# Kernel tuning notes

Hardware: AMD Instinct MI355X
Metric: run time of the kernel (lower is better)

Reference implementation:

```python
import jax, jax.numpy as jnp
import numpy as np

# CogForge GroupedQueryAttention (prefill path): GQA + RoPE + sliding-window+global-token mask
B, T, DM = 2, 2048, 768
H, HKV, DH = 12, 4, 64          # d_head = d_model // n_heads
GROUPS = H // HKV               # kv_groups = 3
WIN, GLB = 512, 64              # window_size, global_tokens
THETA = 10000.0


def _rotate_half(x):
    half = x.shape[-1] // 2
    return jnp.concatenate([-x[..., half:], x[..., :half]], axis=-1)


def _rope_cos_sin(seq_len, dim, dtype):
    inv_freq = 1.0 / (THETA ** (jnp.arange(0, dim, 2, dtype=jnp.float32) / dim))
    t = jnp.arange(seq_len, dtype=jnp.float32)
    freqs = jnp.outer(t, inv_freq)                      # [T, DH/2]
    emb = jnp.concatenate([freqs, freqs], axis=-1)      # [T, DH]
    return jnp.cos(emb).astype(dtype)[None, None], jnp.sin(emb).astype(dtype)[None, None]


def _sparse_mask(seq_len):
    # allowed(i,j) = causal AND (within window OR j is a global token)
    i = jnp.arange(seq_len)[:, None]
    j = jnp.arange(seq_len)[None, :]
    allowed = (j <= i) & (((i - j) < WIN) | (j < GLB))
    return jnp.where(allowed, 0.0, -jnp.inf).astype(jnp.float32)  # [T, T]


def setup_inputs() -> dict:
    key = jax.random.key(0)
    kx, kq, kk, kv, ko = jax.random.split(key, 5)
    x = jax.random.normal(kx, (B, T, DM), jnp.float32)
    wq = jax.random.normal(kq, (DM, H * DH), jnp.float32) * 0.02
    wk = jax.random.normal(kk, (DM, HKV * DH), jnp.float32) * 0.02
    wv = jax.random.normal(kv, (DM, HKV * DH), jnp.float32) * 0.02
    wo = jax.random.normal(ko, (H * DH, DM), jnp.float32) * 0.02
    return {"x": x, "wq": wq, "wk": wk, "wv": wv, "wo": wo}


def reference(x, wq, wk, wv, wo):
    # projections -> [B, heads, T, DH]
    q = (x @ wq).reshape(B, T, H, DH).transpose(0, 2, 1, 3)
    k = (x @ wk).reshape(B, T, HKV, DH).transpose(0, 2, 1, 3)
    v = (x @ wv).reshape(B, T, HKV, DH).transpose(0, 2, 1, 3)

    cos, sin = _rope_cos_sin(T, DH, x.dtype)            # [1,1,T,DH]
    q = q * cos + _rotate_half(q) * sin
    k = k * cos + _rotate_half(k) * sin

    # expand kv heads to match query heads (GQA)
    k = jnp.repeat(k, GROUPS, axis=1)                   # [B,H,T,DH]
    v = jnp.repeat(v, GROUPS, axis=1)

    scale = 1.0 / jnp.sqrt(jnp.asarray(DH, x.dtype))
    scores = jnp.einsum('bhtd,bhsd->bhts', q, k) * scale
    scores = scores + _sparse_mask(T)[None, None]
    weights = jax.nn.softmax(scores, axis=-1)           # attn_dropout = 0.0

    out = jnp.einsum('bhts,bhsd->bhtd', weights, v)
    out = out.transpose(0, 2, 1, 3).reshape(B, T, H * DH)
    return out @ wo
```

## Files before the change

kernel.cpp:

```cpp
#include <hip/hip_runtime.h>
#include <hip/hip_bf16.h>


typedef __attribute__((ext_vector_type(8))) short bf16x8;
typedef __attribute__((ext_vector_type(4))) short bf16x4;
typedef __attribute__((ext_vector_type(4))) float f32x4;
typedef __attribute__((ext_vector_type(4))) unsigned short u16x4;

#define MFMA   __builtin_amdgcn_mfma_f32_16x16x32_bf16
#define MFMA16 __builtin_amdgcn_mfma_f32_16x16x16bf16_1k

constexpr int BB = 2, TT = 2048, DM = 768, HH = 12, HKV = 4, DH = 64;
constexpr int WIN = 512, GLB = 64;
constexpr float SC2 = 0.18033688011112042f;

__device__ __forceinline__ unsigned short f2b(float f) {
    union { float f; unsigned int u; } v; v.f = f;
    unsigned int r = v.u + 0x7fffu + ((v.u >> 16) & 1u);
    return (unsigned short)(r >> 16);
}

#define GLOAD_LDS(gp, lp)                                                      \
    __builtin_amdgcn_global_load_lds(                                          \
        (const __attribute__((address_space(1))) void*)(gp),                   \
        (__attribute__((address_space(3))) void*)(lp), 16, 0, 0)

__global__ __launch_bounds__(256) void k_pre(const float* __restrict__ x,
                                             unsigned short* __restrict__ xb,
                                             float2* __restrict__ rope,
                                             const float* __restrict__ wq,
                                             const float* __restrict__ wk,
                                             const float* __restrict__ wv,
                                             const float* __restrict__ wo,
                                             unsigned short* __restrict__ wqT,
                                             unsigned short* __restrict__ wkT,
                                             unsigned short* __restrict__ wvT,
                                             unsigned short* __restrict__ woT) {
    __shared__ float t[32][33];
    int bid = blockIdx.x, tid = threadIdx.x;
    if (bid < 3072) {
        int i = bid * 256 + tid;
        float4 v = ((const float4*)x)[i];
        u16x4 o; o.x = f2b(v.x); o.y = f2b(v.y); o.z = f2b(v.z); o.w = f2b(v.w);
        ((u16x4*)xb)[i] = o;
        return;
    }
    if (bid < 3328) {
        int i = (bid - 3072) * 256 + tid;
        int tt = i >> 5, p = i & 31;
        float inv = exp2f(-(float)p * (13.287712379549449f / 32.0f));
        float ang = (float)tt * inv;
        rope[i] = make_float2(cosf(ang), sinf(ang));
        return;
    }
    int wb = bid - 3328;
    const float* src; unsigned short* dst; int N, tile;
    if (wb < 576)      { src = wq; dst = wqT; N = 768; tile = wb; }
    else if (wb < 768) { src = wk; dst = wkT; N = 256; tile = wb - 576; }
    else if (wb < 960) { src = wv; dst = wvT; N = 256; tile = wb - 768; }
    else               { src = wo; dst = woT; N = 768; tile = wb - 960; }
    int ntiles = N / 32;
    int k0 = (tile / ntiles) * 32, n0 = (tile % ntiles) * 32;
    int tx = tid & 31, ty = tid >> 5;
    #pragma unroll
    for (int e = 0; e < 4; ++e) {
        int r = ty + e * 8;
        t[r][tx] = src[(size_t)(k0 + r) * N + n0 + tx];
    }
    __syncthreads();
    #pragma unroll
    for (int e = 0; e < 4; ++e) {
        int r = ty + e * 8;
        dst[(size_t)(n0 + r) * DM + k0 + tx] = f2b(t[tx][r]);
    }
}

__global__ __launch_bounds__(256) void k_qkv(const unsigned short* __restrict__ xb,
                                             const unsigned short* __restrict__ wqT,
                                             const unsigned short* __restrict__ wkT,
                                             const unsigned short* __restrict__ wvT,
                                             unsigned short* __restrict__ qb,
                                             unsigned short* __restrict__ kb,
                                             unsigned short* __restrict__ vtb,
                                             const float2* __restrict__ rope) {
    __shared__ __align__(16) unsigned short Ab[2][64 * 64];
    __shared__ __align__(16) unsigned short Bb[2][64 * 64];
    const int tid = threadIdx.x;
    const int wave = tid >> 6, lane = tid & 63;
    const int quad = lane >> 4, col = lane & 15;
    const int y = blockIdx.y;
    int mode, hl;
    const unsigned short* Bt;
    if (y < 12)      { mode = 0; hl = y;      Bt = wqT + (size_t)hl * 64 * DM; }
    else if (y < 16) { mode = 1; hl = y - 12; Bt = wkT + (size_t)hl * 64 * DM; }
    else             { mode = 2; hl = y - 16; Bt = wvT + (size_t)hl * 64 * DM; }
    const int m0b = blockIdx.x * 64;

    const int rg = lane >> 3;
    const int cg = (lane & 7) ^ rg;
    const int ck = col & 7;

    f32x4 acc[4];
    #pragma unroll
    for (int j = 0; j < 4; ++j) acc[j] = f32x4{0.f, 0.f, 0.f, 0.f};

    auto stage = [&](int buf, int k) {
        #pragma unroll
        for (int m = 0; m < 2; ++m) {
            int g = wave * 2 + m;
            GLOAD_LDS(xb + (size_t)(m0b + g * 8 + rg) * DM + k + cg * 8,
                      &Ab[buf][g * 512]);
        }
        #pragma unroll
        for (int m = 0; m < 2; ++m) {
            int g = wave * 2 + m;
            GLOAD_LDS(Bt + (size_t)(g * 8 + rg) * DM + k + cg * 8,
                      &Bb[buf][g * 512]);
        }
    };

    stage(0, 0);
    __syncthreads();

    const int arow = (wave * 16 + col) * 64;

    for (int t = 0; t < 12; ++t) {
        const int buf = t & 1;
        if (t < 11) stage(buf ^ 1, (t + 1) * 64);
        __builtin_amdgcn_s_setprio(1);
        #pragma unroll
        for (int ks = 0; ks < 2; ++ks) {
            const int p = ((ks * 4 + quad) ^ ck) * 8;
            bf16x8 a = *(const bf16x8*)&Ab[buf][arow + p];
            #pragma unroll
            for (int j = 0; j < 4; ++j) {
                bf16x8 b = *(const bf16x8*)&Bb[buf][(j * 16 + col) * 64 + p];
                acc[j] = MFMA(a, b, acc[j], 0, 0, 0);
            }
        }
        __builtin_amdgcn_s_setprio(0);
        __syncthreads();
    }

    if (mode == 2) {
        int b = m0b >> 11;
        #pragma unroll
        for (int j = 0; j < 4; ++j)
            #pragma unroll
            for (int r = 0; r < 4; ++r) {
                int m = m0b + wave * 16 + quad * 4 + r;
                int t = m & (TT - 1);
                int d = j * 16 + col;
                vtb[((size_t)(b * HKV + hl) * DH + d) * TT + t] = f2b(acc[j][r]);
            }
        return;
    }
    int nheads = (mode == 0) ? HH : HKV;
    unsigned short* ob = (mode == 0) ? qb : kb;
    #pragma unroll
    for (int r = 0; r < 4; ++r) {
        int m = m0b + wave * 16 + quad * 4 + r;
        int t = m & (TT - 1);
        int b = m >> 11;
        float2 cs0 = rope[t * 32 + col];
        float2 cs1 = rope[t * 32 + 16 + col];
        float v0 = acc[0][r], v1 = acc[1][r], v2 = acc[2][r], v3 = acc[3][r];
        unsigned short* dst = ob + ((size_t)(b * nheads + hl) * TT + t) * DH + col;
        dst[0]  = f2b(v0 * cs0.x - v2 * cs0.y);
        dst[16] = f2b(v1 * cs1.x - v3 * cs1.y);
        dst[32] = f2b(v2 * cs0.x + v0 * cs0.y);
        dst[48] = f2b(v3 * cs1.x + v1 * cs1.y);
    }
}

__global__ __launch_bounds__(256) void k_out(const unsigned short* __restrict__ ao,
                                             const unsigned short* __restrict__ woT,
                                             float* __restrict__ out) {
    __shared__ __align__(16) unsigned short Ab[2][64 * 64];
    __shared__ __align__(16) unsigned short Bb[2][64 * 64];
    const int tid = threadIdx.x;
    const int wave = tid >> 6, lane = tid & 63;
    const int quad = lane >> 4, col = lane & 15;
    const int m0b = blockIdx.x * 64;
    const int n0 = blockIdx.y * 64;

    const int rg = lane >> 3;
    const int cg = (lane & 7) ^ rg;
    const int ck = col & 7;

    f32x4 acc[4];
    #pragma unroll
    for (int j = 0; j < 4; ++j) acc[j] = f32x4{0.f, 0.f, 0.f, 0.f};

    auto stage = [&](int buf, int k) {
        #pragma unroll
        for (int m = 0; m < 2; ++m) {
            int g = wave * 2 + m;
            GLOAD_LDS(ao + (size_t)(m0b + g * 8 + rg) * DM + k + cg * 8,
                      &Ab[buf][g * 512]);
        }
        #pragma unroll
        for (int m = 0; m < 2; ++m) {
            int g = wave * 2 + m;
            GLOAD_LDS(woT + (size_t)(n0 + g * 8 + rg) * DM + k + cg * 8,
                      &Bb[buf][g * 512]);
        }
    };

    stage(0, 0);
    __syncthreads();

    const int arow = (wave * 16 + col) * 64;

    for (int t = 0; t < 12; ++t) {
        const int buf = t & 1;
        if (t < 11) stage(buf ^ 1, (t + 1) * 64);
        __builtin_amdgcn_s_setprio(1);
        #pragma unroll
        for (int ks = 0; ks < 2; ++ks) {
            const int p = ((ks * 4 + quad) ^ ck) * 8;
            bf16x8 a = *(const bf16x8*)&Ab[buf][arow + p];
            #pragma unroll
            for (int j = 0; j < 4; ++j) {
                bf16x8 b = *(const bf16x8*)&Bb[buf][(j * 16 + col) * 64 + p];
                acc[j] = MFMA(a, b, acc[j], 0, 0, 0);
            }
        }
        __builtin_amdgcn_s_setprio(0);
        __syncthreads();
    }

    #pragma unroll
    for (int j = 0; j < 4; ++j)
        #pragma unroll
        for (int r = 0; r < 4; ++r) {
            int m = m0b + wave * 16 + quad * 4 + r;
            out[(size_t)m * DM + n0 + j * 16 + col] = acc[j][r];
        }
}

__global__ __launch_bounds__(256) void k_attn(const unsigned short* __restrict__ Q,
                                              const unsigned short* __restrict__ K,
                                              const unsigned short* __restrict__ Vt,
                                              unsigned short* __restrict__ AO) {
    __shared__ __align__(16) unsigned short kbuf[2][64 * 64];
    __shared__ __align__(16) unsigned short vbuf[2][64 * 64];
    const int lane = threadIdx.x & 63;
    const int wave = threadIdx.x >> 6;
    const int quad = lane >> 4, col = lane & 15;
    const int lbid = (blockIdx.x & 7) * 96 + (blockIdx.x >> 3);
    const int qb = lbid & 31, bh = lbid >> 5;
    const int h = bh % HH, b = bh / HH;
    const int hkv = h / 3;
    const int i0 = qb * 64 + wave * 16;
    const int irow = i0 + col;

    const unsigned short* qbase = Q + ((size_t)(b * HH + h) * TT + irow) * DH + quad * 8;
    const bf16x8 qf0 = *(const bf16x8*)qbase;
    const bf16x8 qf1 = *(const bf16x8*)(qbase + 32);
    const unsigned short* kbase = K + (size_t)(b * HKV + hkv) * TT * DH;
    const unsigned short* vbase = Vt + (size_t)(b * HKV + hkv) * DH * TT;

    float m_run = -1e30f, l_lane = 0.f;
    f32x4 accO[4];
    #pragma unroll
    for (int dt = 0; dt < 4; ++dt) accO[dt] = f32x4{0.f, 0.f, 0.f, 0.f};

    int jw0 = (qb * 64 - WIN + 1) & ~63; if (jw0 < 64) jw0 = 64;
    const int jlast = qb * 64;
    const int nt = 1 + ((jlast >= 64) ? (((jlast - jw0) >> 6) + 1) : 0);
    auto j0_of = [&](int t) { return (t == 0) ? 0 : (jw0 + ((t - 1) << 6)); };

    const int sr = lane >> 3;
    const int soff = ((lane & 7) ^ sr) * 8;
    const int ck = col & 7;

    auto stage = [&](int bb, int j0) {
        GLOAD_LDS(kbase + (size_t)(j0 + wave * 16 + sr) * DH + soff,
                  &kbuf[bb][(wave * 16) * 64]);
        GLOAD_LDS(kbase + (size_t)(j0 + wave * 16 + 8 + sr) * DH + soff,
                  &kbuf[bb][(wave * 16 + 8) * 64]);
        GLOAD_LDS(vbase + (size_t)(wave * 16 + sr) * TT + j0 + soff,
                  &vbuf[bb][(wave * 16) * 64]);
        GLOAD_LDS(vbase + (size_t)(wave * 16 + 8 + sr) * TT + j0 + soff,
                  &vbuf[bb][(wave * 16 + 8) * 64]);
    };

    stage(0, 0);
    __syncthreads();

    for (int t = 0; t < nt; ++t) {
        const int bb = t & 1;
        if (t + 1 < nt) stage(bb ^ 1, j0_of(t + 1));

        const int j0 = j0_of(t);
        const int mode = (t == 0) ? ((i0 < 64) ? 1 : 0)
                       : (((j0 + 63 > i0) || (j0 <= i0 + 15 - WIN)) ? 2 : 0);

        f32x4 sT[4];
        #pragma unroll
        for (int f = 0; f < 4; ++f) sT[f] = f32x4{0.f, 0.f, 0.f, 0.f};
        __builtin_amdgcn_s_setprio(1);
        #pragma unroll
        for (int f = 0; f < 4; ++f) {
            bf16x8 k0 = *(const bf16x8*)&kbuf[bb][(f * 16 + col) * 64 + (quad ^ ck) * 8];
            bf16x8 k1 = *(const bf16x8*)&kbuf[bb][(f * 16 + col) * 64 + ((4 + quad) ^ ck) * 8];
            sT[f] = MFMA(k0, qf0, sT[f], 0, 0, 0);
            sT[f] = MFMA(k1, qf1, sT[f], 0, 0, 0);
        }
        __builtin_amdgcn_s_setprio(0);

        const int dq = irow - j0 - quad * 4;
        if (mode == 1) {
            #pragma unroll
            for (int f = 0; f < 4; ++f)
                #pragma unroll
                for (int r = 0; r < 4; ++r)
                    if (dq - f * 16 - r < 0) sT[f][r] = -3e30f;
        } else if (mode == 2) {
            #pragma unroll
            for (int f = 0; f < 4; ++f)
                #pragma unroll
                for (int r = 0; r < 4; ++r)
                    if ((unsigned)(dq - f * 16 - r) >= (unsigned)WIN) sT[f][r] = -3e30f;
        }

        float mx = -3e30f;
        #pragma unroll
        for (int f = 0; f < 4; ++f)
            #pragma unroll
            for (int r = 0; r < 4; ++r) mx = fmaxf(mx, sT[f][r]);

        if (!__all(mx <= m_run + 44.f)) {
            float rm = fmaxf(mx, __shfl_xor(mx, 16));
            rm = fmaxf(rm, __shfl_xor(rm, 32));
            float mn = fmaxf(m_run, rm);
            float corr = exp2f((m_run - mn) * SC2);
            m_run = mn;
            l_lane *= corr;
            #pragma unroll
            for (int dt = 0; dt < 4; ++dt)
                #pragma unroll
                for (int r = 0; r < 4; ++r) accO[dt][r] *= corr;
        }

        const float mbase = m_run * SC2;
        unsigned int pk[4][2];
        float ps = 0.f;
        #pragma unroll
        for (int f = 0; f < 4; ++f) {
            float p0 = exp2f(__builtin_fmaf(sT[f][0], SC2, -mbase));
            float p1 = exp2f(__builtin_fmaf(sT[f][1], SC2, -mbase));
            float p2 = exp2f(__builtin_fmaf(sT[f][2], SC2, -mbase));
            float p3 = exp2f(__builtin_fmaf(sT[f][3], SC2, -mbase));
            ps += (p0 + p1) + (p2 + p3);
            asm("v_cvt_pk_bf16_f32 %0, %1, %2" : "=v"(pk[f][0]) : "v"(p0), "v"(p1));
            asm("v_cvt_pk_bf16_f32 %0, %1, %2" : "=v"(pk[f][1]) : "v"(p2), "v"(p3));
        }
        l_lane += ps;

        __builtin_amdgcn_s_setprio(1);
        #pragma unroll
        for (int f = 0; f < 4; ++f) {
            union { bf16x4 v; unsigned int u[2]; } pb;
            pb.u[0] = pk[f][0];
            pb.u[1] = pk[f][1];
            const int voff = (((2 * f + (quad >> 1)) ^ ck) << 3) + ((quad & 1) << 2);
            #pragma unroll
            for (int dt = 0; dt < 4; ++dt) {
                bf16x4 va = *(const bf16x4*)&vbuf[bb][(dt * 16 + col) * 64 + voff];
                accO[dt] = MFMA16(va, pb.v, accO[dt], 0, 0, 0);
            }
        }
        __builtin_amdgcn_s_setprio(0);

        __syncthreads();
    }

    float lr = l_lane;
    lr += __shfl_xor(lr, 16);
    lr += __shfl_xor(lr, 32);
    const float inv = 1.0f / lr;

    unsigned short* dst = AO + ((size_t)b * TT + irow) * DM + h * DH + quad * 4;
    #pragma unroll
    for (int dt = 0; dt < 4; ++dt) {
        u16x4 o;
        o.x = f2b(accO[dt][0] * inv);
        o.y = f2b(accO[dt][1] * inv);
        o.z = f2b(accO[dt][2] * inv);
        o.w = f2b(accO[dt][3] * inv);
        *(u16x4*)(dst + dt * 16) = o;
    }
}

extern "C" void kernel_launch(void* const* d_in, const int* in_sizes, int n_in,
                              void* d_out, int out_size, void* d_ws, size_t ws_size,
                              hipStream_t stream) {
    const float* x  = (const float*)d_in[0];
    const float* wq = (const float*)d_in[1];
    const float* wk = (const float*)d_in[2];
    const float* wv = (const float*)d_in[3];
    const float* wo = (const float*)d_in[4];
    float* out = (float*)d_out;

    char* ws = (char*)d_ws;
    size_t off = 0;
    auto alloc = [&](size_t bytes) -> void* {
        void* p = ws + off;
        off += (bytes + 255) & ~(size_t)255;
        return p;
    };
    const int M = BB * TT;
    unsigned short* xb  = (unsigned short*)alloc((size_t)M * DM * 2);
    unsigned short* wqT = (unsigned short*)alloc((size_t)DM * DM * 2);
    unsigned short* wkT = (unsigned short*)alloc((size_t)(HKV * DH) * DM * 2);
    unsigned short* wvT = (unsigned short*)alloc((size_t)(HKV * DH) * DM * 2);
    unsigned short* woT = (unsigned short*)alloc((size_t)DM * DM * 2);
    unsigned short* qb  = (unsigned short*)alloc((size_t)BB * HH * TT * DH * 2);
    unsigned short* kb  = (unsigned short*)alloc((size_t)BB * HKV * TT * DH * 2);
    unsigned short* vtb = (unsigned short*)alloc((size_t)BB * HKV * DH * TT * 2);
    unsigned short* ao  = (unsigned short*)alloc((size_t)M * DM * 2);
    float2* rope        = (float2*)alloc((size_t)TT * 32 * sizeof(float2));

    k_pre<<<4864, 256, 0, stream>>>(x, xb, rope, wq, wk, wv, wo, wqT, wkT, wvT, woT);
    k_qkv<<<dim3(M / 64, 20), 256, 0, stream>>>(xb, wqT, wkT, wvT, qb, kb, vtb, rope);
    k_attn<<<768, 256, 0, stream>>>(qb, kb, vtb, ao);
    k_out<<<dim3(M / 64, 12), 256, 0, stream>>>(ao, woT, out);
}
```

Measured before the change: 63.89 us.

## Retile QKV and output GEMMs to 128x128 blocks with 2x2 wave grid

New measurement: 75.41 us. 1.18x slower.

```diff
diff --git a/kernel.cpp b/kernel.cpp
--- a/kernel.cpp
+++ b/kernel.cpp
@@ -83,160 +83,165 @@
                                              unsigned short* __restrict__ kb,
                                              unsigned short* __restrict__ vtb,
                                              const float2* __restrict__ rope) {
-    __shared__ __align__(16) unsigned short Ab[2][64 * 64];
-    __shared__ __align__(16) unsigned short Bb[2][64 * 64];
+    __shared__ __align__(16) unsigned short Ab[2][128 * 32];
+    __shared__ __align__(16) unsigned short Bb[2][128 * 32];
     const int tid = threadIdx.x;
     const int wave = tid >> 6, lane = tid & 63;
     const int quad = lane >> 4, col = lane & 15;
+    const int wr = wave >> 1, wc = wave & 1;
     const int y = blockIdx.y;
-    int mode, hl;
+    const int m0b = blockIdx.x * 128;
+    int mode;
     const unsigned short* Bt;
-    if (y < 12)      { mode = 0; hl = y;      Bt = wqT + (size_t)hl * 64 * DM; }
-    else if (y < 16) { mode = 1; hl = y - 12; Bt = wkT + (size_t)hl * 64 * DM; }
-    else             { mode = 2; hl = y - 16; Bt = wvT + (size_t)hl * 64 * DM; }
-    const int m0b = blockIdx.x * 64;
-
-    const int rg = lane >> 3;
-    const int cg = (lane & 7) ^ rg;
-    const int ck = col & 7;
-
-    f32x4 acc[4];
-    #pragma unroll
-    for (int j = 0; j < 4; ++j) acc[j] = f32x4{0.f, 0.f, 0.f, 0.f};
+    int hbase;
+    if (y < 6)      { mode = 0; Bt = wqT + (size_t)(y * 128) * DM;       hbase = y * 2; }
+    else if (y < 8) { mode = 1; Bt = wkT + (size_t)((y - 6) * 128) * DM; hbase = (y - 6) * 2; }
+    else            { mode = 2; Bt = wvT + (size_t)((y - 8) * 128) * DM; hbase = (y - 8) * 2; }
+
+    const int srow = lane >> 2;
+    const int sch  = (lane & 3) * 8;
+
+    f32x4 acc[4][4];
+    #pragma unroll
+    for (int m = 0; m < 4; ++m)
+        #pragma unroll
+        for (int n = 0; n < 4; ++n) acc[m][n] = f32x4{0.f, 0.f, 0.f, 0.f};
 
     auto stage = [&](int buf, int k) {
-        #pragma unroll
-        for (int m = 0; m < 2; ++m) {
-            int g = wave * 2 + m;
-            GLOAD_LDS(xb + (size_t)(m0b + g * 8 + rg) * DM + k + cg * 8,
-                      &Ab[buf][g * 512]);
-        }
-        #pragma unroll
-        for (int m = 0; m < 2; ++m) {
-            int g = wave * 2 + m;
-            GLOAD_LDS(Bt + (size_t)(g * 8 + rg) * DM + k + cg * 8,
-                      &Bb[buf][g * 512]);
-        }
+        GLOAD_LDS(xb + (size_t)(m0b + wave * 32 + srow) * DM + k + sch,
+                  &Ab[buf][(wave * 32) * 32]);
+        GLOAD_LDS(xb + (size_t)(m0b + wave * 32 + 16 + srow) * DM + k + sch,
+                  &Ab[buf][(wave * 32 + 16) * 32]);
+        GLOAD_LDS(Bt + (size_t)(wave * 32 + srow) * DM + k + sch,
+                  &Bb[buf][(wave * 32) * 32]);
+        GLOAD_LDS(Bt + (size_t)(wave * 32 + 16 + srow) * DM + k + sch,
+                  &Bb[buf][(wave * 32 + 16) * 32]);
     };
 
     stage(0, 0);
     __syncthreads();
 
-    const int arow = (wave * 16 + col) * 64;
-
-    for (int t = 0; t < 12; ++t) {
+    for (int t = 0; t < 24; ++t) {
         const int buf = t & 1;
-        if (t < 11) stage(buf ^ 1, (t + 1) * 64);
+        if (t < 23) stage(buf ^ 1, (t + 1) * 32);
         __builtin_amdgcn_s_setprio(1);
-        #pragma unroll
-        for (int ks = 0; ks < 2; ++ks) {
-            const int p = ((ks * 4 + quad) ^ ck) * 8;
-            bf16x8 a = *(const bf16x8*)&Ab[buf][arow + p];
-            #pragma unroll
-            for (int j = 0; j < 4; ++j) {
-                bf16x8 b = *(const bf16x8*)&Bb[buf][(j * 16 + col) * 64 + p];
-                acc[j] = MFMA(a, b, acc[j], 0, 0, 0);
-            }
-        }
+        bf16x8 af[4], bf[4];
+        #pragma unroll
+        for (int m = 0; m < 4; ++m)
+            af[m] = *(const bf16x8*)&Ab[buf][(wr * 64 + m * 16 + col) * 32 + quad * 8];
+        #pragma unroll
+        for (int n = 0; n < 4; ++n)
+            bf[n] = *(const bf16x8*)&Bb[buf][(wc * 64 + n * 16 + col) * 32 + quad * 8];
+        #pragma unroll
+        for (int m = 0; m < 4; ++m)
+            #pragma unroll
+            for (int n = 0; n < 4; ++n)
+                acc[m][n] = MFMA(af[m], bf[n], acc[m][n], 0, 0, 0);
         __builtin_amdgcn_s_setprio(0);
         __syncthreads();
     }
 
+    const int hl = hbase + wc;
     if (mode == 2) {
-        int b = m0b >> 11;
-        #pragma unroll
-        for (int j = 0; j < 4; ++j)
-            #pragma unroll
-            for (int r = 0; r < 4; ++r) {
-                int m = m0b + wave * 16 + quad * 4 + r;
-                int t = m & (TT - 1);
-                int d = j * 16 + col;
-                vtb[((size_t)(b * HKV + hl) * DH + d) * TT + t] = f2b(acc[j][r]);
-            }
+        #pragma unroll
+        for (int m = 0; m < 4; ++m)
+            #pragma unroll
+            for (int n = 0; n < 4; ++n)
+                #pragma unroll
+                for (int r = 0; r < 4; ++r) {
+                    int row = m0b + wr * 64 + m * 16 + quad * 4 + r;
+                    int t = row & (TT - 1);
+                    int b = row >> 11;
+                    int d = n * 16 + col;
+                    vtb[((size_t)(b * HKV + hl) * DH + d) * TT + t] = f2b(acc[m][n][r]);
+                }
         return;
     }
     int nheads = (mode == 0) ? HH : HKV;
     unsigned short* ob = (mode == 0) ? qb : kb;
     #pragma unroll
-    for (int r = 0; r < 4; ++r) {
-        int m = m0b + wave * 16 + quad * 4 + r;
-        int t = m & (TT - 1);
-        int b = m >> 11;
-        float2 cs0 = rope[t * 32 + col];
-        float2 cs1 = rope[t * 32 + 16 + col];
-        float v0 = acc[0][r], v1 = acc[1][r], v2 = acc[2][r], v3 = acc[3][r];
-        unsigned short* dst = ob + ((size_t)(b * nheads + hl) * TT + t) * DH + col;
-        dst[0]  = f2b(v0 * cs0.x - v2 * cs0.y);
-        dst[16] = f2b(v1 * cs1.x - v3 * cs1.y);
-        dst[32] = f2b(v2 * cs0.x + v0 * cs0.y);
-        dst[48] = f2b(v3 * cs1.x + v1 * cs1.y);
-    }
+    for (int m = 0; m < 4; ++m)
+        #pragma unroll
+        for (int r = 0; r < 4; ++r) {
+            int row = m0b + wr * 64 + m * 16 + quad * 4 + r;
+            int t = row & (TT - 1);
+            int b = row >> 11;
+            float2 cs0 = rope[t * 32 + col];
+            float2 cs1 = rope[t * 32 + 16 + col];
+            float v0 = acc[m][0][r], v1 = acc[m][1][r], v2 = acc[m][2][r], v3 = acc[m][3][r];
+            unsigned short* dst = ob + ((size_t)(b * nheads + hl) * TT + t) * DH + col;
+            dst[0]  = f2b(v0 * cs0.x - v2 * cs0.y);
+            dst[16] = f2b(v1 * cs1.x - v3 * cs1.y);
+            dst[32] = f2b(v2 * cs0.x + v0 * cs0.y);
+            dst[48] = f2b(v3 * cs1.x + v1 * cs1.y);
+        }
 }
 
 __global__ __launch_bounds__(256) void k_out(const unsigned short* __restrict__ ao,
                                              const unsigned short* __restrict__ woT,
                                              float* __restrict__ out) {
-    __shared__ __align__(16) unsigned short Ab[2][64 * 64];
-    __shared__ __align__(16) unsigned short Bb[2][64 * 64];
+    __shared__ __align__(16) unsigned short Ab[2][128 * 32];
+    __shared__ __align__(16) unsigned short Bb[2][128 * 32];
     const int tid = threadIdx.x;
     const int wave = tid >> 6, lane = tid & 63;
     const int quad = lane >> 4, col = lane & 15;
-    const int m0b = blockIdx.x * 64;
-    const int n0 = blockIdx.y * 64;
-
-    const int rg = lane >> 3;
-    const int cg = (lane & 7) ^ rg;
-    const int ck = col & 7;
-
-    f32x4 acc[4];
-    #pragma unroll
-    for (int j = 0; j < 4; ++j) acc[j] = f32x4{0.f, 0.f, 0.f, 0.f};
+    const int wr = wave >> 1, wc = wave & 1;
+    const int m0b = blockIdx.x * 128;
+    const int n0b = blockIdx.y * 128;
+    const unsigned short* Bt = woT + (size_t)n0b * DM;
+
+    const int srow = lane >> 2;
+    const int sch  = (lane & 3) * 8;
+
+    f32x4 acc[4][4];
+    #pragma unroll
+    for (int m = 0; m < 4; ++m)
+        #pragma unroll
+        for (int n = 0; n < 4; ++n) acc[m][n] = f32x4{0.f, 0.f, 0.f, 0.f};
 
     auto stage = [&](int buf, int k) {
-        #pragma unroll
-        for (int m = 0; m < 2; ++m) {
-            int g = wave * 2 + m;
-            GLOAD_LDS(ao + (size_t)(m0b + g * 8 + rg) * DM + k + cg * 8,
-                      &Ab[buf][g * 512]);
-        }
-        #pragma unroll
-        for (int m = 0; m < 2; ++m) {
-            int g = wave * 2 + m;
-            GLOAD_LDS(woT + (size_t)(n0 + g * 8 + rg) * DM + k + cg * 8,
-                      &Bb[buf][g * 512]);
-        }
+        GLOAD_LDS(ao + (size_t)(m0b + wave * 32 + srow) * DM + k + sch,
+                  &Ab[buf][(wave * 32) * 32]);
+        GLOAD_LDS(ao + (size_t)(m0b + wave * 32 + 16 + srow) * DM + k + sch,
+                  &Ab[buf][(wave * 32 + 16) * 32]);
+        GLOAD_LDS(Bt + (size_t)(wave * 32 + srow) * DM + k + sch,
+                  &Bb[buf][(wave * 32) * 32]);
+        GLOAD_LDS(Bt + (size_t)(wave * 32 + 16 + srow) * DM + k + sch,
+                  &Bb[buf][(wave * 32 + 16) * 32]);
     };
 
     stage(0, 0);
     __syncthreads();
 
-    const int arow = (wave * 16 + col) * 64;
-
-    for (int t = 0; t < 12; ++t) {
+    for (int t = 0; t < 24; ++t) {
         const int buf = t & 1;
-        if (t < 11) stage(buf ^ 1, (t + 1) * 64);
+        if (t < 23) stage(buf ^ 1, (t + 1) * 32);
         __builtin_amdgcn_s_setprio(1);
-        #pragma unroll
-        for (int ks = 0; ks < 2; ++ks) {
-            const int p = ((ks * 4 + quad) ^ ck) * 8;
-            bf16x8 a = *(const bf16x8*)&Ab[buf][arow + p];
-            #pragma unroll
-            for (int j = 0; j < 4; ++j) {
-                bf16x8 b = *(const bf16x8*)&Bb[buf][(j * 16 + col) * 64 + p];
-                acc[j] = MFMA(a, b, acc[j], 0, 0, 0);
-            }
-        }
+        bf16x8 af[4], bf[4];
+        #pragma unroll
+        for (int m = 0; m < 4; ++m)
+            af[m] = *(const bf16x8*)&Ab[buf][(wr * 64 + m * 16 + col) * 32 + quad * 8];
+        #pragma unroll
+        for (int n = 0; n < 4; ++n)
+            bf[n] = *(const bf16x8*)&Bb[buf][(wc * 64 + n * 16 + col) * 32 + quad * 8];
+        #pragma unroll
+        for (int m = 0; m < 4; ++m)
+            #pragma unroll
+            for (int n = 0; n < 4; ++n)
+                acc[m][n] = MFMA(af[m], bf[n], acc[m][n], 0, 0, 0);
         __builtin_amdgcn_s_setprio(0);
         __syncthreads();
     }
 
     #pragma unroll
-    for (int j = 0; j < 4; ++j)
-        #pragma unroll
-        for (int r = 0; r < 4; ++r) {
-            int m = m0b + wave * 16 + quad * 4 + r;
-            out[(size_t)m * DM + n0 + j * 16 + col] = acc[j][r];
-        }
+    for (int m = 0; m < 4; ++m)
+        #pragma unroll
+        for (int n = 0; n < 4; ++n)
+            #pragma unroll
+            for (int r = 0; r < 4; ++r) {
+                int row = m0b + wr * 64 + m * 16 + quad * 4 + r;
+                out[(size_t)row * DM + n0b + wc * 64 + n * 16 + col] = acc[m][n][r];
+            }
 }
 
 __global__ __launch_bounds__(256) void k_attn(const unsigned short* __restrict__ Q,
@@ -424,7 +429,7 @@
     float2* rope        = (float2*)alloc((size_t)TT * 32 * sizeof(float2));
 
     k_pre<<<4864, 256, 0, stream>>>(x, xb, rope, wq, wk, wv, wo, wqT, wkT, wvT, woT);
-    k_qkv<<<dim3(M / 64, 20), 256, 0, stream>>>(xb, wqT, wkT, wvT, qb, kb, vtb, rope);
+    k_qkv<<<dim3(32, 10), 256, 0, stream>>>(xb, wqT, wkT, wvT, qb, kb, vtb, rope);
     k_attn<<<768, 256, 0, stream>>>(qb, kb, vtb, ao);
-    k_out<<<dim3(M / 64, 12), 256, 0, stream>>>(ao, woT, out);
-}
+    k_out<<<dim3(32, 6), 256, 0, stream>>>(ao, woT, out);
+}
```
